# Kernel optimization log

Measured on AMD Instinct MI355X. Metric: run time of the kernel, lower is better.

Reference implementation:

```python
import jax, jax.numpy as jnp
import numpy as np

D, NH, NL, NP, DFF = 256, 8, 4, 4, 1024
DH = D // NH
# 4-level FPN of a 1024x1024 image at strides 8/16/32/64 (H, W per level)
SHAPES = np.array([[128, 128], [64, 64], [32, 32], [16, 16]], dtype=np.int32)


def setup_inputs() -> dict:
    ks = jax.random.split(jax.random.key(0), 16)
    B, Lq = 4, 900
    sizes = SHAPES[:, 0] * SHAPES[:, 1]
    Lin = int(sizes.sum())
    starts = np.concatenate([[0], np.cumsum(sizes)[:-1]]).astype(np.int32)
    s = 0.02  # small init so softmax/LN stay well-conditioned

    def w(k, shape):
        return jax.random.normal(k, shape, jnp.float32) * s

    return {
        "tgt": jax.random.normal(ks[0], (Lq, B, D), jnp.float32),
        "tgt_reference_points": jax.random.uniform(ks[1], (Lq, B, NL, 2), jnp.float32),
        "memory": jax.random.normal(ks[2], (Lin, B, D), jnp.float32),
        "W_off": w(ks[3], (NH * NL * NP * 2, D)), "b_off": w(ks[4], (NH * NL * NP * 2,)),
        "W_attn": w(ks[5], (NH * NL * NP, D)), "b_attn": w(ks[6], (NH * NL * NP,)),
        "W_val": w(ks[7], (D, D)), "b_val": w(ks[8], (D,)),
        "W_out": w(ks[9], (D, D)), "b_out": w(ks[10], (D,)),
        "ln1_g": jnp.ones((D,), jnp.float32), "ln1_b": jnp.zeros((D,), jnp.float32),
        "W1": w(ks[11], (DFF, D)), "b1": w(ks[12], (DFF,)),
        "W2": w(ks[13], (D, DFF)), "b2": w(ks[14], (D,)),
        "ln3_g": jnp.ones((D,), jnp.float32), "ln3_b": jnp.zeros((D,), jnp.float32),
        "memory_spatial_shapes": jnp.asarray(SHAPES),
        "memory_level_start_index": jnp.asarray(starts),
        "memory_key_padding_mask": jnp.zeros((B, Lin), jnp.bool_),
    }


def _ln(x, g, b, eps=1e-5):
    mu = x.mean(-1, keepdims=True)
    var = ((x - mu) ** 2).mean(-1, keepdims=True)
    return (x - mu) * jax.lax.rsqrt(var + eps) * g + b


def _bilinear(vl, loc, H, W):
    # vl: (B, NH, H*W, DH); loc: (B, Lq, NH, NP, 2) normalized to [0,1]
    # matches torch grid_sample(mode='bilinear', padding_mode='zeros', align_corners=False)
    B, Lq, nh, P, _ = loc.shape
    x = loc[..., 0] * W - 0.5
    y = loc[..., 1] * H - 0.5
    x0f = jnp.floor(x)
    y0f = jnp.floor(y)
    x0 = x0f.astype(jnp.int32)
    y0 = y0f.astype(jnp.int32)
    wx1 = x - x0f
    wy1 = y - y0f

    def tap(xi, yi, w):
        valid = (xi >= 0) & (xi < W) & (yi >= 0) & (yi < H)
        idx = jnp.clip(yi, 0, H - 1) * W + jnp.clip(xi, 0, W - 1)
        idx = idx.transpose(0, 2, 1, 3).reshape(B, nh, Lq * P)
        ww = (w * valid).transpose(0, 2, 1, 3).reshape(B, nh, Lq * P)
        vals = jnp.take_along_axis(vl, idx[..., None], axis=2)  # (B,NH,Lq*P,DH)
        return vals * ww[..., None]

    acc = (tap(x0, y0, (1 - wx1) * (1 - wy1)) + tap(x0 + 1, y0, wx1 * (1 - wy1))
           + tap(x0, y0 + 1, (1 - wx1) * wy1) + tap(x0 + 1, y0 + 1, wx1 * wy1))
    return acc.reshape(B, nh, Lq, P, DH)


def _msda(q, ref, value, shapes_np, W_off, b_off, W_attn, b_attn, W_out, b_out):
    # q: (B,Lq,D), ref: (B,Lq,NL,2), value: (B,Lin,NH,DH)
    B, Lq, _ = q.shape
    off = (q @ W_off.T + b_off).reshape(B, Lq, NH, NL, NP, 2)
    a = jax.nn.softmax((q @ W_attn.T + b_attn).reshape(B, Lq, NH, NL * NP), axis=-1)
    a = a.reshape(B, Lq, NH, NL, NP)
    norm = jnp.asarray(shapes_np[:, ::-1].copy(), jnp.float32)  # (NL, 2) as (W, H)
    loc = ref[:, :, None, :, None, :] + off / norm[None, None, None, :, None, :]
    sizes = [int(h) * int(w) for h, w in shapes_np]
    starts = np.concatenate([[0], np.cumsum(sizes)[:-1]])
    v = value.transpose(0, 2, 1, 3)  # (B, NH, Lin, DH)
    out = jnp.zeros((B, NH, Lq, DH), q.dtype)
    for l, (H, W) in enumerate(shapes_np):
        vl = v[:, :, int(starts[l]):int(starts[l]) + sizes[l], :]
        sampled = _bilinear(vl, loc[:, :, :, l], int(H), int(W))  # (B,NH,Lq,NP,DH)
        wl = a[:, :, :, l].transpose(0, 2, 1, 3)  # (B,NH,Lq,NP)
        out = out + (sampled * wl[..., None]).sum(3)
    out = out.transpose(0, 2, 1, 3).reshape(B, Lq, D)
    return out @ W_out.T + b_out


def reference(tgt, tgt_reference_points, memory, W_off, b_off, W_attn, b_attn,
              W_val, b_val, W_out, b_out, ln1_g, ln1_b, W1, b1, W2, b2, ln3_g, ln3_b,
              memory_spatial_shapes, memory_level_start_index, memory_key_padding_mask):
    shapes_np = np.asarray(memory_spatial_shapes)  # static level metadata
    q = tgt.transpose(1, 0, 2)                      # (B, Lq, D)
    ref = tgt_reference_points.transpose(1, 0, 2, 3)
    mem = memory.transpose(1, 0, 2)                 # (B, Lin, D)
    B, Lin, _ = mem.shape
    value = mem @ W_val.T + b_val
    value = jnp.where(memory_key_padding_mask[..., None], 0.0, value)
    value = value.reshape(B, Lin, NH, DH)
    ca = _msda(q, ref, value, shapes_np, W_off, b_off, W_attn, b_attn, W_out, b_out)
    # residual + LN (dropout is identity in eval)
    t = _ln(tgt + ca.transpose(1, 0, 2), ln1_g, ln1_b)
    # FFN
    t2 = jax.nn.relu(t @ W1.T + b1) @ W2.T + b2
    return _ln(t + t2, ln3_g, ln3_b)
```

## Files before the change

kernel.cpp:

```cpp
#include <hip/hip_runtime.h>
#include <hip/hip_bf16.h>

#define B_   4
#define LQ_  900
#define D_   256
#define NH_  8
#define DH_  32
#define NL_  4
#define NP_  4
#define DFF_ 1024
#define LIN_ 21760
#define MQ_  (LQ_*B_)
#define MV_  (LIN_*B_)
#define VALBLKS ((MV_/32)*2)

typedef __attribute__((ext_vector_type(8))) short bh8;
typedef __attribute__((ext_vector_type(4))) float f32x4;

__device__ __forceinline__ short bf16b(float f) {
    __hip_bfloat16 h = __float2bfloat16(f);
    return *reinterpret_cast<short*>(&h);
}

__device__ __forceinline__ void gload_lds16(const void* g, void* l) {
    __builtin_amdgcn_global_load_lds(
        (const __attribute__((address_space(1))) unsigned int*)g,
        (__attribute__((address_space(3))) unsigned int*)l, 16, 0, 0);
}

__device__ __forceinline__ bh8 af_from_f32(const float* p) {
    float4 v0 = *reinterpret_cast<const float4*>(p);
    float4 v1 = *reinterpret_cast<const float4*>(p + 4);
    return (bh8){ bf16b(v0.x), bf16b(v0.y), bf16b(v0.z), bf16b(v0.w),
                  bf16b(v1.x), bf16b(v1.y), bf16b(v1.z), bf16b(v1.w) };
}

__global__ __launch_bounds__(256)
void wprep_k(const float* __restrict__ Woff, const float* __restrict__ Wattn,
             const float* __restrict__ Wout, const float* __restrict__ W1,
             const float* __restrict__ W2, const float* __restrict__ Wval,
             unsigned char* __restrict__ qkvimg, unsigned char* __restrict__ outimg,
             unsigned char* __restrict__ w1img, unsigned char* __restrict__ w2img,
             unsigned char* __restrict__ valimg)
{
    const int cid = blockIdx.x*256 + threadIdx.x;
    const float* W; unsigned char* img; int KQ, c;
    if      (cid < 8192)  { W=Woff;  img=qkvimg;           KQ=8;  c=cid;       }
    else if (cid < 12288) { W=Wattn; img=qkvimg + 131072;  KQ=8;  c=cid-8192;  }
    else if (cid < 20480) { W=Wout;  img=outimg;           KQ=8;  c=cid-12288; }
    else if (cid < 53248) { W=W1;    img=w1img;            KQ=8;  c=cid-20480; }
    else if (cid < 86016) { W=W2;    img=w2img;            KQ=32; c=cid-53248; }
    else                  { W=Wval;  img=valimg;           KQ=8;  c=cid-86016; }
    const int K   = KQ*32;
    const int n16 = c & 15, g = (c>>4)&3, t = c>>6;
    const int kq  = t & (KQ-1);
    const int ntile = t >> ((KQ==8) ? 3 : 5);
    const int n = ntile*16 + n16, k0 = kq*32 + g*8;
    float4 v0 = *reinterpret_cast<const float4*>(&W[(size_t)n*K + k0]);
    float4 v1 = *reinterpret_cast<const float4*>(&W[(size_t)n*K + k0 + 4]);
    union { short s[8]; uint4 u; } pk;
    pk.s[0]=bf16b(v0.x); pk.s[1]=bf16b(v0.y); pk.s[2]=bf16b(v0.z); pk.s[3]=bf16b(v0.w);
    pk.s[4]=bf16b(v1.x); pk.s[5]=bf16b(v1.y); pk.s[6]=bf16b(v1.z); pk.s[7]=bf16b(v1.w);
    *reinterpret_cast<uint4*>(img + (size_t)(ntile*KQ + kq)*1024 + (g*16+n16)*16) = pk.u;
}

__global__ __launch_bounds__(256, 4)
void valqkv_k(const float* __restrict__ A, const unsigned char* __restrict__ Wimg,
              const float* __restrict__ bias, unsigned short* __restrict__ C,
              const unsigned char* __restrict__ mask,
              const float* __restrict__ tgt, const unsigned char* __restrict__ Qimg,
              const float* __restrict__ b_off, const float* __restrict__ b_attn,
              float* __restrict__ Yoff, float* __restrict__ Yattn)
{
    __shared__ __align__(16) unsigned char Al[32768];

    const int tid  = threadIdx.x;
    const int lane = tid & 63;

    if (blockIdx.x < VALBLKS) {
        const int wc    = tid >> 6;
        const int mt    = blockIdx.x >> 1;
        const int nhalf = blockIdx.x & 1;
        const int m0    = mt * 32;
        const int r16   = lane & 15;
        const int g     = lane >> 4;

        const unsigned char* Abyte = (const unsigned char*)A;
        const unsigned char* wlane = Wimg + lane*16;

        const int a_row = (tid >> 3) & 31;
        const int a_x   = (tid & 7) * 16;
        const size_t a_src_row = (size_t)(m0 + a_row) * 1024 + (a_x ^ ((a_row & 7) << 4));
        const int a_dst = tid * 16;

#define ISSUE_A(KQ) gload_lds16(Abyte + a_src_row + (KQ)*128, (char*)Al + (KQ)*4096 + a_dst)

        bh8 wreg[2][8];
        #pragma unroll
        for (int i = 0; i < 2; ++i)
            #pragma unroll
            for (int kq = 0; kq < 8; ++kq)
                wreg[i][kq] = *reinterpret_cast<const bh8*>(
                    wlane + (size_t)((nhalf*8 + wc*2 + i)*8 + kq)*1024);

        ISSUE_A(0);
        ISSUE_A(1);
        ISSUE_A(2);

        asm volatile("s_waitcnt vmcnt(3)" ::: "memory");
        #pragma unroll
        for (int i = 0; i < 2; ++i)
            #pragma unroll
            for (int kq = 0; kq < 8; ++kq)
                asm volatile("" : "+v"(wreg[i][kq]));

        f32x4 acc[2][2];
        #pragma unroll
        for (int i = 0; i < 2; ++i)
            #pragma unroll
            for (int j = 0; j < 2; ++j) acc[i][j] = (f32x4){0.f,0.f,0.f,0.f};

        #pragma unroll
        for (int kq = 0; kq < 8; ++kq) {
            if (kq < 6)      asm volatile("s_waitcnt vmcnt(2)" ::: "memory");
            else if (kq == 6) asm volatile("s_waitcnt vmcnt(1)" ::: "memory");
            else              asm volatile("s_waitcnt vmcnt(0)" ::: "memory");
            __builtin_amdgcn_s_barrier();

            bh8 af[2];
            #pragma unroll
            for (int mf = 0; mf < 2; ++mf) {
                const int row = mf*16 + r16;
                const int swz = (row & 7) << 4;
                const char* base = (const char*)Al + kq*4096 + row*128;
                float4 v0 = *reinterpret_cast<const float4*>(base + ((g*32     ) ^ swz));
                float4 v1 = *reinterpret_cast<const float4*>(base + ((g*32 + 16) ^ swz));
                af[mf] = (bh8){ bf16b(v0.x), bf16b(v0.y), bf16b(v0.z), bf16b(v0.w),
                                bf16b(v1.x), bf16b(v1.y), bf16b(v1.z), bf16b(v1.w) };
            }

            if (kq < 5) ISSUE_A(kq + 3);

            #pragma unroll
            for (int mf = 0; mf < 2; ++mf)
                #pragma unroll
                for (int i = 0; i < 2; ++i)
                    acc[mf][i] = __builtin_amdgcn_mfma_f32_16x16x32_bf16(af[mf], wreg[i][kq], acc[mf][i], 0, 0, 0);
        }
#undef ISSUE_A

        float bv[2];
        #pragma unroll
        for (int i = 0; i < 2; ++i) bv[i] = bias[nhalf*128 + wc*32 + i*16 + r16];

        #pragma unroll
        for (int mf = 0; mf < 2; ++mf) {
            #pragma unroll
            for (int r = 0; r < 4; ++r) {
                const int gm = m0 + mf*16 + g*4 + r;
                const bool z = mask[(gm & 3)*LIN_ + (gm >> 2)] != 0;
                #pragma unroll
                for (int i = 0; i < 2; ++i) {
                    float v = acc[mf][i][r] + bv[i];
                    if (z) v = 0.f;
                    C[(size_t)gm*256 + nhalf*128 + wc*32 + i*16 + r16] = (unsigned short)bf16b(v);
                }
            }
        }
    } else {
        const int w   = tid >> 6;
        const int m16 = lane & 15, g = lane >> 4;
        const int m0  = (blockIdx.x - VALBLKS) * 16;

        bh8 af[8];
        #pragma unroll
        for (int kq = 0; kq < 8; ++kq)
            af[kq] = af_from_f32(&tgt[(size_t)(m0 + m16)*256 + kq*32 + g*8]);

        f32x4 acc[6];
        #pragma unroll
        for (int i = 0; i < 6; ++i) acc[i] = (f32x4){0.f,0.f,0.f,0.f};

        #pragma unroll
        for (int i = 0; i < 6; ++i) {
            const int nt = w*6 + i;
            #pragma unroll
            for (int kq = 0; kq < 8; ++kq) {
                bh8 bf = *reinterpret_cast<const bh8*>(Qimg + (size_t)(nt*8 + kq)*1024 + lane*16);
                acc[i] = __builtin_amdgcn_mfma_f32_16x16x32_bf16(af[kq], bf, acc[i], 0, 0, 0);
            }
        }

        #pragma unroll
        for (int i = 0; i < 6; ++i) {
            const int nt = w*6 + i;
            const int j  = nt*16 + m16;
            #pragma unroll
            for (int r = 0; r < 4; ++r) {
                const int m = m0 + g*4 + r;
                if (nt < 16) Yoff[(size_t)m*256 + j] = acc[i][r] + b_off[j];
                else         Yattn[(size_t)m*128 + (j-256)] = acc[i][r] + b_attn[j-256];
            }
        }
    }
}

__global__ __launch_bounds__(1024, 2)
void outffn_k(const float* __restrict__ Amsda, const unsigned char* __restrict__ Oimg,
              const float* __restrict__ b_out, const float* __restrict__ res,
              const float* __restrict__ l1g, const float* __restrict__ l1b,
              const unsigned char* __restrict__ W1img, const float* __restrict__ b1,
              const unsigned char* __restrict__ W2img, const float* __restrict__ b2,
              const float* __restrict__ l3g, const float* __restrict__ l3b,
              float* __restrict__ Yout)
{
    __shared__ float sln[16][256];
    __shared__ __align__(16) short hl[2][16*272];

    const int tid = threadIdx.x, lane = tid & 63, w = tid >> 6;
    const int m16 = lane & 15, g = lane >> 4;
    const int m0 = blockIdx.x * 16;

    {
        bh8 af[8];
        #pragma unroll
        for (int kq = 0; kq < 8; ++kq)
            af[kq] = af_from_f32(&Amsda[(size_t)(m0 + m16)*256 + kq*32 + g*8]);

        f32x4 acc = (f32x4){0.f,0.f,0.f,0.f};
        #pragma unroll
        for (int kq = 0; kq < 8; ++kq) {
            bh8 bf = *reinterpret_cast<const bh8*>(Oimg + (size_t)(w*8 + kq)*1024 + lane*16);
            acc = __builtin_amdgcn_mfma_f32_16x16x32_bf16(af[kq], bf, acc, 0, 0, 0);
        }

        const int j = w*16 + m16;
        #pragma unroll
        for (int r = 0; r < 4; ++r) {
            const int ml = g*4 + r;
            sln[ml][j] = acc[r] + b_out[j] + res[(size_t)(m0 + ml)*256 + j];
        }
    }
    __syncthreads();

    {
        const int row = w, l2 = lane;
        float v[4], s1 = 0.f, s2 = 0.f;
        #pragma unroll
        for (int c = 0; c < 4; ++c) {
            v[c] = sln[row][l2 + c*64];
            s1 += v[c]; s2 += v[c]*v[c];
        }
        #pragma unroll
        for (int o = 32; o >= 1; o >>= 1) {
            s1 += __shfl_xor(s1, o, 64);
            s2 += __shfl_xor(s2, o, 64);
        }
        const float mu  = s1 * (1.f/256.f);
        const float var = s2 * (1.f/256.f) - mu*mu;
        const float is  = rsqrtf(var + 1e-5f);
        #pragma unroll
        for (int c = 0; c < 4; ++c) {
            const int jj = l2 + c*64;
            sln[row][jj] = (v[c] - mu) * is * l1g[jj] + l1b[jj];
        }
    }
    __syncthreads();

    bh8 af1[8];
    #pragma unroll
    for (int kq = 0; kq < 8; ++kq)
        af1[kq] = af_from_f32(&sln[m16][kq*32 + g*8]);

    f32x4 yacc = (f32x4){0.f,0.f,0.f,0.f};

    int buf = 0;
    #pragma unroll
    for (int fc = 0; fc < 4; ++fc) {
        const int ftile_g = fc*16 + w;
        f32x4 hacc = (f32x4){0.f,0.f,0.f,0.f};
        #pragma unroll
        for (int kq = 0; kq < 8; ++kq) {
            bh8 bf = *reinterpret_cast<const bh8*>(W1img + (size_t)(ftile_g*8 + kq)*1024 + lane*16);
            hacc = __builtin_amdgcn_mfma_f32_16x16x32_bf16(af1[kq], bf, hacc, 0, 0, 0);
        }
        const float bb = b1[ftile_g*16 + m16];
        #pragma unroll
        for (int r = 0; r < 4; ++r) {
            const float v = fmaxf(hacc[r] + bb, 0.f);
            hl[buf][(g*4 + r)*272 + w*16 + m16] = bf16b(v);
        }
        __syncthreads();
        bh8 a2[8];
        #pragma unroll
        for (int kqf = 0; kqf < 8; ++kqf)
            a2[kqf] = *reinterpret_cast<const bh8*>((const char*)&hl[buf][0]
                + m16*544 + (kqf*32 + g*8)*2);
        #pragma unroll
        for (int kqf = 0; kqf < 8; ++kqf) {
            const int kq2 = fc*8 + kqf;
            bh8 bf = *reinterpret_cast<const bh8*>(W2img + (size_t)(w*32 + kq2)*1024 + lane*16);
            yacc = __builtin_amdgcn_mfma_f32_16x16x32_bf16(a2[kqf], bf, yacc, 0, 0, 0);
        }
        buf ^= 1;
    }

    {
        const int j = w*16 + m16;
        #pragma unroll
        for (int r = 0; r < 4; ++r) {
            const int ml = g*4 + r;
            sln[ml][j] = yacc[r] + b2[j] + sln[ml][j];
        }
    }
    __syncthreads();

    {
        const int row = w, l2 = lane;
        float v[4], s1 = 0.f, s2 = 0.f;
        #pragma unroll
        for (int c = 0; c < 4; ++c) {
            v[c] = sln[row][l2 + c*64];
            s1 += v[c]; s2 += v[c]*v[c];
        }
        #pragma unroll
        for (int o = 32; o >= 1; o >>= 1) {
            s1 += __shfl_xor(s1, o, 64);
            s2 += __shfl_xor(s2, o, 64);
        }
        const float mu  = s1 * (1.f/256.f);
        const float var = s2 * (1.f/256.f) - mu*mu;
        const float is  = rsqrtf(var + 1e-5f);
        #pragma unroll
        for (int c = 0; c < 4; ++c) {
            const int jj = l2 + c*64;
            Yout[(size_t)(m0 + row)*256 + jj] = (v[c] - mu) * is * l3g[jj] + l3b[jj];
        }
    }
}

__global__ __launch_bounds__(256)
void msda_k(const float* __restrict__ off,
            const float* __restrict__ attnlog,
            const float* __restrict__ refp,
            const __hip_bfloat16* __restrict__ value,
            float* __restrict__ out)
{
    const int hp = threadIdx.x >> 7;
    const int dd = threadIdx.x & 127;
    const int d0 = dd * 2;
    const int m  = blockIdx.x*2 + hp;
    const int b  = m & 3;
    const int h  = dd >> 4;

    __shared__ float s_off[2][256];
    __shared__ float s_al[2][128];
    __shared__ float s_ref[2][NL_*2];
    {
        const int t2 = threadIdx.x & 127;
        s_off[hp][t2]       = off[(size_t)m*256 + t2];
        s_off[hp][t2 + 128] = off[(size_t)m*256 + t2 + 128];
        if (t2 < 128) s_al[hp][t2] = attnlog[(size_t)m*128 + t2];
        if (t2 < NL_*2) s_ref[hp][t2] = refp[(size_t)m*(NL_*2) + t2];
    }
    __syncthreads();

    float mx = -1e30f;
    #pragma unroll
    for (int t = 0; t < 16; ++t) mx = fmaxf(mx, s_al[hp][h*16 + t]);
    float e[16], ssum = 0.f;
    #pragma unroll
    for (int t = 0; t < 16; ++t) { e[t] = __expf(s_al[hp][h*16 + t] - mx); ssum += e[t]; }
    const float inv = 1.f / ssum;

    const int HS[4] = {128, 64, 32, 16};
    const int ST[4] = {0, 16384, 20480, 21504};

    float acc0 = 0.f, acc1 = 0.f;
    #pragma unroll
    for (int l = 0; l < NL_; ++l) {
        const int H = HS[l], W = HS[l], st = ST[l];
        const float rx = s_ref[hp][l*2+0], ry = s_ref[hp][l*2+1];
        #pragma unroll
        for (int p = 0; p < NP_; ++p) {
            const int base = ((h*NL_ + l)*NP_ + p);
            const float a  = e[l*4 + p] * inv;
            const float ox = s_off[hp][base*2+0], oy = s_off[hp][base*2+1];
            const float x = rx*(float)W + ox - 0.5f;
            const float y = ry*(float)H + oy - 0.5f;
            const float x0f = floorf(x), y0f = floorf(y);
            const int x0 = (int)x0f, y0 = (int)y0f;
            const float wx1 = x - x0f, wy1 = y - y0f;
            const float wx0 = 1.f - wx1, wy0 = 1.f - wy1;
            #pragma unroll
            for (int t = 0; t < 4; ++t) {
                const int xi = x0 + (t & 1);
                const int yi = y0 + (t >> 1);
                const float wgt = (t==0 ? wx0*wy0 : t==1 ? wx1*wy0 : t==2 ? wx0*wy1 : wx1*wy1);
                if (xi >= 0 && xi < W && yi >= 0 && yi < H) {
                    const size_t idx = (size_t)(st + yi*W + xi);
                    const unsigned int v = *reinterpret_cast<const unsigned int*>(
                        &value[(idx*B_ + b)*D_ + d0]);
                    const float f0 = __uint_as_float(v << 16);
                    const float f1 = __uint_as_float(v & 0xffff0000u);
                    const float aw = a * wgt;
                    acc0 = fmaf(aw, f0, acc0);
                    acc1 = fmaf(aw, f1, acc1);
                }
            }
        }
    }
    float2 o2 = { acc0, acc1 };
    *reinterpret_cast<float2*>(&out[(size_t)m*256 + d0]) = o2;
}

extern "C" void kernel_launch(void* const* d_in, const int* in_sizes, int n_in,
                              void* d_out, int out_size, void* d_ws, size_t ws_size,
                              hipStream_t stream)
{
    const float* tgt    = (const float*)d_in[0];
    const float* refp   = (const float*)d_in[1];
    const float* mem    = (const float*)d_in[2];
    const float* W_off  = (const float*)d_in[3];
    const float* b_off  = (const float*)d_in[4];
    const float* W_attn = (const float*)d_in[5];
    const float* b_attn = (const float*)d_in[6];
    const float* W_val  = (const float*)d_in[7];
    const float* b_val  = (const float*)d_in[8];
    const float* W_out  = (const float*)d_in[9];
    const float* b_out  = (const float*)d_in[10];
    const float* ln1g   = (const float*)d_in[11];
    const float* ln1b   = (const float*)d_in[12];
    const float* W1     = (const float*)d_in[13];
    const float* b1     = (const float*)d_in[14];
    const float* W2     = (const float*)d_in[15];
    const float* b2     = (const float*)d_in[16];
    const float* ln3g   = (const float*)d_in[17];
    const float* ln3b   = (const float*)d_in[18];
    const unsigned char* mask = (const unsigned char*)d_in[21];
    float* out = (float*)d_out;

    char* p = (char*)d_ws;
    __hip_bfloat16* value = (__hip_bfloat16*)p; p += (size_t)MV_*D_*2;
    float* offb = (float*)p; p += (size_t)MQ_*256*4;
    float* attl = (float*)p; p += (size_t)MQ_*128*4;
    float* msda = (float*)p; p += (size_t)MQ_*256*4;
    unsigned char* qkvimg = (unsigned char*)p; p += 196608;
    unsigned char* outimg = (unsigned char*)p; p += 131072;
    unsigned char* w1img  = (unsigned char*)p; p += 524288;
    unsigned char* w2img  = (unsigned char*)p; p += 524288;
    unsigned char* valimg = (unsigned char*)p; p += 131072;
    (void)ws_size; (void)in_sizes; (void)n_in; (void)out_size;

    wprep_k<<<dim3(368), dim3(256), 0, stream>>>(W_off, W_attn, W_out, W1, W2, W_val,
                                                 qkvimg, outimg, w1img, w2img, valimg);
    valqkv_k<<<dim3(VALBLKS + MQ_/16), dim3(256), 0, stream>>>(
        mem, valimg, b_val, (unsigned short*)value, mask,
        tgt, qkvimg, b_off, b_attn, offb, attl);
    msda_k<<<dim3(MQ_/2), dim3(256), 0, stream>>>(offb, attl, refp, value, msda);
    outffn_k<<<dim3(MQ_/16), dim3(1024), 0, stream>>>(
        msda, outimg, b_out, tgt, ln1g, ln1b,
        w1img, b1, w2img, b2, ln3g, ln3b, out);
}
```

Before: 112.1 us.

## Stage value-projection weights in LDS instead of registers in valqkv kernel

The value-projection GEMM path now copies each block's 64KB bf16 weight half into shared memory with async global-to-LDS loads, instead of holding it in per-lane registers. The A-tile buffer shrinks to a 4-slot ring indexed modulo 4. Launch bounds drop from 4 to 2 blocks per CU to fit the larger shared-memory footprint. The aim is to cut register pressure and overlap the weight fetch with A loads, at the cost of lower occupancy and extra LDS reads per MFMA step.

```diff
diff --git a/kernel.cpp b/kernel.cpp
--- a/kernel.cpp
+++ b/kernel.cpp
@@ -64,7 +64,7 @@
     *reinterpret_cast<uint4*>(img + (size_t)(ntile*KQ + kq)*1024 + (g*16+n16)*16) = pk.u;
 }
 
-__global__ __launch_bounds__(256, 4)
+__global__ __launch_bounds__(256, 2)
 void valqkv_k(const float* __restrict__ A, const unsigned char* __restrict__ Wimg,
               const float* __restrict__ bias, unsigned short* __restrict__ C,
               const unsigned char* __restrict__ mask,
@@ -72,7 +72,8 @@
               const float* __restrict__ b_off, const float* __restrict__ b_attn,
               float* __restrict__ Yoff, float* __restrict__ Yattn)
 {
-    __shared__ __align__(16) unsigned char Al[32768];
+    __shared__ __align__(16) unsigned char Wl[65536];
+    __shared__ __align__(16) unsigned char Al[16384];
 
     const int tid  = threadIdx.x;
     const int lane = tid & 63;
@@ -86,33 +87,23 @@
         const int g     = lane >> 4;
 
         const unsigned char* Abyte = (const unsigned char*)A;
-        const unsigned char* wlane = Wimg + lane*16;
 
         const int a_row = (tid >> 3) & 31;
         const int a_x   = (tid & 7) * 16;
         const size_t a_src_row = (size_t)(m0 + a_row) * 1024 + (a_x ^ ((a_row & 7) << 4));
         const int a_dst = tid * 16;
 
-#define ISSUE_A(KQ) gload_lds16(Abyte + a_src_row + (KQ)*128, (char*)Al + (KQ)*4096 + a_dst)
-
-        bh8 wreg[2][8];
-        #pragma unroll
-        for (int i = 0; i < 2; ++i)
-            #pragma unroll
-            for (int kq = 0; kq < 8; ++kq)
-                wreg[i][kq] = *reinterpret_cast<const bh8*>(
-                    wlane + (size_t)((nhalf*8 + wc*2 + i)*8 + kq)*1024);
-
+#define ISSUE_A(KQ) gload_lds16(Abyte + a_src_row + (KQ)*128, (char*)Al + ((KQ)&3)*4096 + a_dst)
+
+        {
+            const unsigned char* wsrc = Wimg + (size_t)nhalf*65536;
+            #pragma unroll
+            for (int c = 0; c < 16; ++c)
+                gload_lds16(wsrc + c*4096 + tid*16, (char*)Wl + c*4096 + tid*16);
+        }
         ISSUE_A(0);
         ISSUE_A(1);
         ISSUE_A(2);
-
-        asm volatile("s_waitcnt vmcnt(3)" ::: "memory");
-        #pragma unroll
-        for (int i = 0; i < 2; ++i)
-            #pragma unroll
-            for (int kq = 0; kq < 8; ++kq)
-                asm volatile("" : "+v"(wreg[i][kq]));
 
         f32x4 acc[2][2];
         #pragma unroll
@@ -132,7 +123,7 @@
             for (int mf = 0; mf < 2; ++mf) {
                 const int row = mf*16 + r16;
                 const int swz = (row & 7) << 4;
-                const char* base = (const char*)Al + kq*4096 + row*128;
+                const char* base = (const char*)Al + (kq & 3)*4096 + row*128;
                 float4 v0 = *reinterpret_cast<const float4*>(base + ((g*32     ) ^ swz));
                 float4 v1 = *reinterpret_cast<const float4*>(base + ((g*32 + 16) ^ swz));
                 af[mf] = (bh8){ bf16b(v0.x), bf16b(v0.y), bf16b(v0.z), bf16b(v0.w),
@@ -142,10 +133,14 @@
             if (kq < 5) ISSUE_A(kq + 3);
 
             #pragma unroll
-            for (int mf = 0; mf < 2; ++mf)
+            for (int i = 0; i < 2; ++i) {
+                const int ntl = wc*2 + i;
+                bh8 bf = *reinterpret_cast<const bh8*>(
+                    (const char*)Wl + (ntl*8 + kq)*1024 + lane*16);
                 #pragma unroll
-                for (int i = 0; i < 2; ++i)
-                    acc[mf][i] = __builtin_amdgcn_mfma_f32_16x16x32_bf16(af[mf], wreg[i][kq], acc[mf][i], 0, 0, 0);
+                for (int mf = 0; mf < 2; ++mf)
+                    acc[mf][i] = __builtin_amdgcn_mfma_f32_16x16x32_bf16(af[mf], bf, acc[mf][i], 0, 0, 0);
+            }
         }
 #undef ISSUE_A
 
```

Measured after the change: 122.3 us. 9.1% more time.
